# Kernel tuning notes

Measured on AMD Instinct MI355X. Metric: run time of the kernel, lower is better.

Reference implementation:

```python
import jax, jax.numpy as jnp
import numpy as np

B, N, E = 8, 1000, 16000
HIST, PRED = 8, 12
IN_DIM = 14          # pm25(1) + met features(13)
HID_GAT, HEADS = 256, 8
GNN_OUT = 13
HID = 64             # GRU hidden (self.hid_dim = 64 in source)


def setup_inputs() -> dict:
    key = jax.random.key(0)
    ks = jax.random.split(key, 20)
    p = lambda k, shp, s=0.05: jax.random.normal(k, shp, dtype=jnp.float32) * s
    return {
        "pm25_hist": jax.random.normal(ks[0], (B, HIST, N, 1), dtype=jnp.float32),
        "feature": jax.random.normal(ks[1], (B, HIST + PRED, N, IN_DIM - 1), dtype=jnp.float32),
        "edge_index": jax.random.randint(ks[2], (2, E), 0, N),
        "gat1_W": p(ks[3], (IN_DIM, HEADS * HID_GAT)),
        "gat1_att_src": p(ks[4], (HEADS, HID_GAT)),
        "gat1_att_dst": p(ks[5], (HEADS, HID_GAT)),
        "gat1_b": p(ks[6], (HEADS * HID_GAT,)),
        "gat2_W": p(ks[7], (HEADS * HID_GAT, GNN_OUT)),
        "gat2_att_src": p(ks[8], (1, GNN_OUT)),
        "gat2_att_dst": p(ks[9], (1, GNN_OUT)),
        "gat2_b": p(ks[10], (GNN_OUT,)),
        "gru_W_ih": p(ks[11], (3 * HID, IN_DIM + GNN_OUT)),
        "gru_W_hh": p(ks[12], (3 * HID, HID)),
        "gru_b_ih": p(ks[13], (3 * HID,)),
        "gru_b_hh": p(ks[14], (3 * HID,)),
        "fc_out_W": p(ks[15], (HID, 1)),
        "fc_out_b": p(ks[16], (1,)),
    }


def _gat_conv(x, W, a_src, a_dst, b, src, dst, concat):
    # Single-graph GATConv (PyG semantics, eval mode: dropout disabled).
    # x: [N, F_in]; src/dst: [E'] (self-loops already appended)
    H, D = a_src.shape
    h = (x @ W).reshape(N, H, D)                       # [N, H, D]
    e = jax.nn.leaky_relu(
        (h * a_src).sum(-1)[src] + (h * a_dst).sum(-1)[dst], 0.2
    )                                                  # [E', H]
    # segment softmax over incoming edges of each dst node
    m = jax.ops.segment_max(e, dst, num_segments=N)
    ex = jnp.exp(e - m[dst])
    alpha = ex / jax.ops.segment_sum(ex, dst, num_segments=N)[dst]
    out = jax.ops.segment_sum(alpha[:, :, None] * h[src], dst, num_segments=N)  # [N, H, D]
    return (out.reshape(N, H * D) + b) if concat else (out.mean(1) + b)


def reference(pm25_hist, feature, edge_index,
              gat1_W, gat1_att_src, gat1_att_dst, gat1_b,
              gat2_W, gat2_att_src, gat2_att_dst, gat2_b,
              gru_W_ih, gru_W_hh, gru_b_ih, gru_b_hh,
              fc_out_W, fc_out_b):
    # add self-loops (PyG GATConv default)
    loop = jnp.arange(N)
    src = jnp.concatenate([edge_index[0], loop])
    dst = jnp.concatenate([edge_index[1], loop])

    def gnn(x):  # x: [N, IN_DIM] -> [N, GNN_OUT]
        h = jax.nn.elu(_gat_conv(x, gat1_W, gat1_att_src, gat1_att_dst, gat1_b, src, dst, True))
        return _gat_conv(h, gat2_W, gat2_att_src, gat2_att_dst, gat2_b, src, dst, False)

    gnn_b = jax.vmap(gnn)

    def gru(x, h):  # torch.nn.GRUCell math
        i_r, i_z, i_n = jnp.split(x @ gru_W_ih.T + gru_b_ih, 3, axis=-1)
        h_r, h_z, h_n = jnp.split(h @ gru_W_hh.T + gru_b_hh, 3, axis=-1)
        r = jax.nn.sigmoid(i_r + h_r)
        z = jax.nn.sigmoid(i_z + h_z)
        n = jnp.tanh(i_n + r * h_n)
        return (1.0 - z) * n + z * h

    feats = jnp.moveaxis(feature[:, HIST:HIST + PRED], 1, 0)  # [PRED, B, N, 13]

    def step(carry, f_t):
        hn, xn = carry
        x = jnp.concatenate([xn, f_t], axis=-1)               # [B, N, IN_DIM]
        g = gnn_b(x)                                          # [B, N, GNN_OUT]
        gx = jnp.concatenate([g, x], axis=-1).reshape(B * N, IN_DIM + GNN_OUT)
        hn = gru(gx, hn)                                      # [B*N, HID]
        xn = hn.reshape(B, N, HID) @ fc_out_W + fc_out_b      # [B, N, 1]
        return (hn, xn), xn

    h0 = jnp.zeros((B * N, HID), jnp.float32)
    xn0 = pm25_hist[:, -1]                                    # [B, N, 1]
    _, preds = jax.lax.scan(step, (h0, xn0), feats)
    return jnp.moveaxis(preds, 0, 1)                          # [B, PRED, N, 1]
```

## Files before the change

### kernel.cpp

```cpp
#include <hip/hip_runtime.h>
#include <hip/hip_bf16.h>
#include <math.h>

#define BB 8
#define NN 1000
#define EE 16000
#define ETOT 17000
#define TPRED 12
#define FEAT 13
#define INDIM 14
#define HEADS 8
#define HG 256
#define C1 2048
#define GO 13
#define HID 64

typedef unsigned int  uint32;
typedef unsigned short ushort16;
typedef uint32 uvec4 __attribute__((ext_vector_type(4)));
typedef __fp16 hf2 __attribute__((ext_vector_type(2)));

union U32H2 { uint32 u; hf2 h; };
__device__ __forceinline__ hf2 u2h(uint32 u){ U32H2 c; c.u=u; return c.h; }
__device__ __forceinline__ uint32 h2u(hf2 h){ U32H2 c; c.h=h; return c.u; }

#if __has_builtin(__builtin_amdgcn_fdot2)
__device__ __forceinline__ float FDOT2(hf2 a, hf2 b, float c){
    return __builtin_amdgcn_fdot2(a, b, c, false);
}
#else
__device__ __forceinline__ float FDOT2(hf2 a, hf2 b, float c){
    return c + (float)a.x*(float)b.x + (float)a.y*(float)b.y;
}
#endif

__device__ __forceinline__ float lrelu(float v){ return v > 0.f ? v : 0.2f*v; }

__device__ __forceinline__ ushort16 f2bf(float f){
    union { float f; uint32 u; } v; v.f = f;
    uint32 r = v.u + 0x7FFFu + ((v.u >> 16) & 1u);
    return (ushort16)(r >> 16);
}
__device__ __forceinline__ uint32 pack2(float lo, float hi){
    return (uint32)f2bf(lo) | ((uint32)f2bf(hi) << 16);
}
__device__ __forceinline__ void cvt2(uint32 u, float& lo, float& hi){
    union { uint32 u; float f; } a, b;
    a.u = u << 16; b.u = u & 0xFFFF0000u;
    lo = a.f; hi = b.f;
}
__device__ __forceinline__ uint32 pkh(float lo, float hi){
    hf2 h; h.x = (__fp16)lo; h.y = (__fp16)hi; return h2u(h);
}

__global__ void k_prep(const float* W1, const float* a1s, const float* a1d,
                       const float* W2, const float* a2s, const float* a2d,
                       const float* Wih, const float* Whh,
                       float* Wsrc, float* Wdst, uint32* w1pk, uint32* w2pk,
                       uint32* WihP, uint32* WhhP){
    __shared__ float rs[4], rd[4];
    int bid = blockIdx.x, tid = threadIdx.x;
    if (bid < 112){
        int k = bid >> 3, h = bid & 7;
        float wv = W1[k*C1 + h*HG + tid];
        float ps = wv * a1s[h*HG + tid];
        float pd = wv * a1d[h*HG + tid];
        #pragma unroll
        for (int m=1;m<64;m<<=1){ ps += __shfl_xor(ps,m); pd += __shfl_xor(pd,m); }
        int w = tid>>6;
        if ((tid&63)==0){ rs[w]=ps; rd[w]=pd; }
        __syncthreads();
        if (tid==0){
            Wsrc[k*8+h] = rs[0]+rs[1]+rs[2]+rs[3];
            Wdst[k*8+h] = rd[0]+rd[1]+rd[2]+rd[3];
        }
    } else if (bid < 176){
        int i = (bid-112)*256 + tid;
        int c = i >> 3, kk = i & 7;
        float lo = (kk < 7) ? W1[(2*kk)*C1 + c]   : 0.f;
        float hi = (kk < 7) ? W1[(2*kk+1)*C1 + c] : 0.f;
        w1pk[i] = h2u(__builtin_amdgcn_cvt_pkrtz(lo, hi));
    } else if (bid < 180){
        int m = (bid-176)*256 + tid;
        if (m < C1/2){
            int c0 = 2*m, c1 = 2*m+1;
            float colA[16], colB[16];
            float ssA=0.f, ddA=0.f, ssB=0.f, ddB=0.f;
            #pragma unroll
            for (int j=0;j<GO;j++){
                float wA = W2[c0*GO+j], wB = W2[c1*GO+j];
                colA[j]=wA; colB[j]=wB;
                ssA += wA*a2s[j]; ddA += wA*a2d[j];
                ssB += wB*a2s[j]; ddB += wB*a2d[j];
            }
            colA[13]=ssA; colA[14]=ddA; colA[15]=0.f;
            colB[13]=ssB; colB[14]=ddB; colB[15]=0.f;
            #pragma unroll
            for (int j=0;j<16;j++)
                w2pk[m*16+j] = h2u(__builtin_amdgcn_cvt_pkrtz(colA[j], colB[j]));
        }
    } else {
        int i = (bid-180)*256 + tid;
        if (i < 192*14){
            int rr = i/14, c2 = i - rr*14;
            float lo = Wih[rr*27 + 2*c2];
            float hi = (2*c2+1 < 27) ? Wih[rr*27 + 2*c2 + 1] : 0.f;
            WihP[i] = pkh(lo, hi);
        }
        if (i < 192*32){
            int rr = i>>5, j2 = i&31;
            WhhP[i] = pkh(Whh[rr*64 + 2*j2], Whh[rr*64 + 2*j2 + 1]);
        }
    }
}

__global__ void k_init(const float* pm25, const float* feat,
                       const float* Wsrc, const float* Wdst,
                       float* hn, float* xn, int* count,
                       float* ssrc, float* sdst, uint32* xpk){
    int i = blockIdx.x*blockDim.x + threadIdx.x;
    if (i < BB*NN*HID) hn[i] = 0.f;
    if (i < NN) count[i] = 0;
    if (i < BB*NN){
        int b = i/NN, n = i%NN;
        float x[INDIM];
        x[0] = pm25[(b*8 + 7)*NN + n];
        xn[i] = x[0];
        const float* fp = feat + ((size_t)(b*20 + 8)*NN + n)*FEAT;
        #pragma unroll
        for (int k=0;k<FEAT;k++) x[k+1] = fp[k];
        #pragma unroll
        for (int h=0;h<8;h++){
            float ss=0.f, dd=0.f;
            #pragma unroll
            for (int k=0;k<INDIM;k++){ ss += x[k]*Wsrc[k*8+h]; dd += x[k]*Wdst[k*8+h]; }
            ssrc[i*8+h] = ss; sdst[i*8+h] = dd;
        }
        #pragma unroll
        for (int p=0;p<7;p++) xpk[i*8+p] = pack2(x[2*p], x[2*p+1]);
        xpk[i*8+7] = 0u;
    }
}

__global__ void k_count(const int* ei, int* count){
    int e = blockIdx.x*blockDim.x + threadIdx.x;
    if (e < ETOT){
        int dst = (e<EE) ? ei[EE+e] : (e-EE);
        atomicAdd(&count[dst], 1);
    }
}

__global__ void k_scan(const int* count, int* offs, int* cursor){
    __shared__ int s[1024];
    int tid = threadIdx.x;
    int myc = (tid<NN) ? count[tid] : 0;
    s[tid] = myc;
    __syncthreads();
    for (int d=1; d<1024; d<<=1){
        int v = (tid>=d) ? s[tid-d] : 0;
        __syncthreads();
        s[tid] += v;
        __syncthreads();
    }
    if (tid<NN){
        int off = s[tid] - myc;
        offs[tid] = off; cursor[tid] = off;
    }
    if (tid==NN-1) offs[NN] = s[tid];
}

__global__ void k_fill(const int* ei, int* cursor, int* csr_src){
    int e = blockIdx.x*blockDim.x + threadIdx.x;
    if (e < ETOT){
        int src = (e<EE) ? ei[e]    : (e-EE);
        int dst = (e<EE) ? ei[EE+e] : (e-EE);
        int pos = atomicAdd(&cursor[dst], 1);
        csr_src[pos] = src;
    }
}


__global__ __launch_bounds__(256) void k_gnn(const uint32* xpk, const float* ssrc,
        const float* sdst, const int* offs, const int* csr,
        const uint32* w1pk, const uint32* w2pk, const float* b1,
        float* h2o, float* s2s, float* s2d){
    int tid = threadIdx.x;
    int w = tid >> 6, lane = tid & 63;
    int hh = tid >> 5;
    uint32 w1r[64];
    #pragma unroll
    for (int q=0;q<16;q++){
        uvec4 u = *(const uvec4*)(w1pk + tid*64 + 4*q);
        w1r[4*q]=u.x; w1r[4*q+1]=u.y; w1r[4*q+2]=u.z; w1r[4*q+3]=u.w;
    }
    uint32 w2r[64];
    #pragma unroll
    for (int q=0;q<16;q++){
        uvec4 u = *(const uvec4*)(w2pk + tid*64 + 4*q);
        w2r[4*q]=u.x; w2r[4*q+1]=u.y; w2r[4*q+2]=u.z; w2r[4*q+3]=u.w;
    }
    float b1r[8];
    #pragma unroll
    for (int j=0;j<8;j++) b1r[j] = b1[8*tid+j];
    __shared__ float aggL[4][128];
    __shared__ float sred[256*17];
    __shared__ float red2[64];
    for (int rr=0; rr<4; rr++){
        int nid = rr*2048 + w*512 + blockIdx.x;
        if (nid < BB*NN){
            int b = nid & 7, dstn = nid >> 3;
            int bn = b*NN + dstn;
            int base = offs[dstn], deg = offs[dstn+1]-base;
            int slot = lane >> 3, h = lane & 7;
            float sdd = sdst[bn*8 + h];
            float mloc = -1e30f;
            for (int i=slot;i<deg;i+=8){
                int s = csr[base+i];
                mloc = fmaxf(mloc, lrelu(ssrc[(b*NN+s)*8+h]+sdd));
            }
            mloc = fmaxf(mloc, __shfl_xor(mloc,8));
            mloc = fmaxf(mloc, __shfl_xor(mloc,16));
            mloc = fmaxf(mloc, __shfl_xor(mloc,32));
            float dloc = 0.f;
            for (int i=slot;i<deg;i+=8){
                int s = csr[base+i];
                dloc += __expf(lrelu(ssrc[(b*NN+s)*8+h]+sdd)-mloc);
            }
            dloc += __shfl_xor(dloc,8); dloc += __shfl_xor(dloc,16); dloc += __shfl_xor(dloc,32);
            float rden = 1.f/dloc;
            float acc[14];
            #pragma unroll
            for (int k=0;k<14;k++) acc[k]=0.f;
            for (int i=slot;i<deg;i+=8){
                int s = csr[base+i];
                float al = __expf(lrelu(ssrc[(b*NN+s)*8+h]+sdd)-mloc)*rden;
                const uint32* xp = xpk + (size_t)(b*NN+s)*8;
                #pragma unroll
                for (int p=0;p<7;p++){
                    float x0,x1; cvt2(xp[p],x0,x1);
                    acc[2*p]   += al*x0;
                    acc[2*p+1] += al*x1;
                }
            }
            #pragma unroll
            for (int k=0;k<14;k++){
                acc[k] += __shfl_xor(acc[k],8);
                acc[k] += __shfl_xor(acc[k],16);
                acc[k] += __shfl_xor(acc[k],32);
            }
            if (slot==0){
                float* ag = &aggL[w][h*16];
                #pragma unroll
                for (int k=0;k<14;k++) ag[k] = acc[k];
            }
        }
        __syncthreads();
        #pragma unroll
        for (int i=0;i<4;i++){
            int nid2 = rr*2048 + i*512 + blockIdx.x;
            if (nid2 < BB*NN){
                int b2i = nid2 & 7, d2 = nid2 >> 3;
                int bn2 = b2i*NN + d2;
                const float4* ap = (const float4*)(&aggL[i][hh*16]);
                float4 A0=ap[0], A1=ap[1], A2=ap[2], A3=ap[3];
                hf2 agh[7];
                agh[0]=__builtin_amdgcn_cvt_pkrtz(A0.x,A0.y);
                agh[1]=__builtin_amdgcn_cvt_pkrtz(A0.z,A0.w);
                agh[2]=__builtin_amdgcn_cvt_pkrtz(A1.x,A1.y);
                agh[3]=__builtin_amdgcn_cvt_pkrtz(A1.z,A1.w);
                agh[4]=__builtin_amdgcn_cvt_pkrtz(A2.x,A2.y);
                agh[5]=__builtin_amdgcn_cvt_pkrtz(A2.z,A2.w);
                agh[6]=__builtin_amdgcn_cvt_pkrtz(A3.x,A3.y);
                float v[8];
                #pragma unroll
                for (int j=0;j<8;j++){
                    float s = b1r[j];
                    #pragma unroll
                    for (int kk=0;kk<7;kk++) s = FDOT2(agh[kk], u2h(w1r[j*8+kk]), s);
                    v[j] = s > 0.f ? s : __expf(s) - 1.f;
                }
                hf2 vp[4];
                #pragma unroll
                for (int q=0;q<4;q++) vp[q] = __builtin_amdgcn_cvt_pkrtz(v[2*q], v[2*q+1]);
                #pragma unroll
                for (int j=0;j<16;j++){
                    float s = 0.f;
                    #pragma unroll
                    for (int q=0;q<4;q++) s = FDOT2(vp[q], u2h(w2r[q*16+j]), s);
                    sred[tid*17 + j] = s;
                }
                __syncthreads();
                int j = tid & 15, g = tid >> 4;
                float s = 0.f;
                #pragma unroll
                for (int q=0;q<16;q++) s += sred[(g + 16*q)*17 + j];
                s += __shfl_xor(s, 16);
                s += __shfl_xor(s, 32);
                int ww = tid >> 6, ll = tid & 63;
                if (ll < 16) red2[ww*16 + ll] = s;
                __syncthreads();
                if (tid < 15){
                    float rv = red2[tid] + red2[16+tid] + red2[32+tid] + red2[48+tid];
                    if (tid < GO)      h2o[bn2*GO + tid] = rv;
                    else if (tid==13)  s2s[bn2] = rv;
                    else               s2d[bn2] = rv;
                }
                __syncthreads();
            }
        }
        __syncthreads();
    }
}

__global__ __launch_bounds__(64,2) void k_tail(int t, int last,
        const float* feat, const int* offs, const int* csr,
        const float* h2, const float* s2src, const float* s2dst, const float* b2,
        const uint32* WihP, const uint32* WhhP, const float* bih, const float* bhh,
        const float* fcw, const float* fcb, const float* Wsrc, const float* Wdst,
        float* hn, float* xn, float* out,
        float* ssrc, float* sdst, uint32* xpk){
    int lane = threadIdx.x;
    int slot = lane >> 4, cc = lane & 15;
    uint32 wih0[14], wih1[14], wih2[14];
    #pragma unroll
    for (int q=0;q<14;q++){
        wih0[q]=WihP[lane*14+q];
        wih1[q]=WihP[(64+lane)*14+q];
        wih2[q]=WihP[(128+lane)*14+q];
    }
    uint32 whh0[32], whh1[32], whh2[32];
    #pragma unroll
    for (int q=0;q<32;q++){
        whh0[q]=WhhP[lane*32+q];
        whh1[q]=WhhP[(64+lane)*32+q];
        whh2[q]=WhhP[(128+lane)*32+q];
    }
    float bi0=bih[lane], bi1=bih[64+lane], bi2=bih[128+lane];
    float bh0=bhh[lane], bh1=bhh[64+lane], bh2=bhh[128+lane];
    float fw = fcw[lane], fb = fcb[0];
    float b2c = b2[cc < GO ? cc : 0];
    __shared__ uint32 hsP[32];
    __shared__ float garr[14];
    for (int r=0;r<4;r++){
        int bn = blockIdx.x*4 + r;
        int b = bn/NN, n = bn - b*NN;
        int base = offs[n], deg = offs[n+1]-base;
        float sdd = s2dst[bn];
        float mloc = -1e30f;
        for (int e=slot;e<deg;e+=4){
            int s = csr[base+e];
            mloc = fmaxf(mloc, lrelu(s2src[b*NN+s] + sdd));
        }
        mloc = fmaxf(mloc, __shfl_xor(mloc,16));
        mloc = fmaxf(mloc, __shfl_xor(mloc,32));
        float dloc = 0.f;
        for (int e=slot;e<deg;e+=4){
            int s = csr[base+e];
            dloc += __expf(lrelu(s2src[b*NN+s] + sdd) - mloc);
        }
        dloc += __shfl_xor(dloc,16);
        dloc += __shfl_xor(dloc,32);
        float rdv = 1.f / dloc;
        float a = 0.f;
        for (int e=slot;e<deg;e+=4){
            int s = csr[base+e];
            float al = __expf(lrelu(s2src[b*NN+s] + sdd) - mloc) * rdv;
            a += al * h2[(size_t)(b*NN+s)*GO + cc];
        }
        a += __shfl_xor(a,16);
        a += __shfl_xor(a,32);
        float xnv = xn[bn];
        if (slot==0 && cc<GO)  garr[cc] = a + b2c;
        if (slot==0 && cc==GO) garr[GO] = xnv;
        float hold = hn[bn*HID + lane];
        if (lane<32) hsP[lane] = pkh(hn[bn*HID + 2*lane], hn[bn*HID + 2*lane + 1]);
        __syncthreads();
        const float* fp = feat + ((size_t)(b*20 + 8 + t)*NN + n)*FEAT;
        float ft[FEAT];
        #pragma unroll
        for (int k=0;k<FEAT;k++) ft[k] = fp[k];
        hf2 gx[14];
        #pragma unroll
        for (int p=0;p<7;p++) gx[p] = u2h(pkh(garr[2*p], garr[2*p+1]));
        #pragma unroll
        for (int p=0;p<6;p++) gx[7+p] = u2h(pkh(ft[2*p], ft[2*p+1]));
        gx[13] = u2h(pkh(ft[12], 0.f));
        float ir = bi0, iz = bi1, inn = bi2;
        #pragma unroll
        for (int c2=0;c2<14;c2++){
            ir  = FDOT2(gx[c2], u2h(wih0[c2]), ir);
            iz  = FDOT2(gx[c2], u2h(wih1[c2]), iz);
            inn = FDOT2(gx[c2], u2h(wih2[c2]), inn);
        }
        float hr = bh0, hz = bh1, hnv = bh2;
        #pragma unroll
        for (int j2=0;j2<32;j2++){
            hf2 hv = u2h(hsP[j2]);
            hr  = FDOT2(hv, u2h(whh0[j2]), hr);
            hz  = FDOT2(hv, u2h(whh1[j2]), hz);
            hnv = FDOT2(hv, u2h(whh2[j2]), hnv);
        }
        float rg = 1.f/(1.f+__expf(-(ir+hr)));
        float zg = 1.f/(1.f+__expf(-(iz+hz)));
        float nv = tanhf(inn + rg*hnv);
        float hnew = (1.f - zg)*nv + zg*hold;
        hn[bn*HID+lane] = hnew;
        float xv = hnew * fw;
        #pragma unroll
        for (int m=1;m<64;m<<=1) xv += __shfl_xor(xv,m);
        float res = xv + fb;
        if (lane==0){
            xn[bn] = res;
            out[(b*TPRED + t)*NN + n] = res;
        }
        if (!last){
            const float* fp2 = feat + ((size_t)(b*20 + 9 + t)*NN + n)*FEAT;
            if (lane < 16){
                int h = lane & 7;
                const float* Wa = (lane<8) ? Wsrc : Wdst;
                float s = res * Wa[h];
                #pragma unroll
                for (int k=1;k<14;k++) s += fp2[k-1]*Wa[k*8+h];
                if (lane<8) ssrc[bn*8+h] = s; else sdst[bn*8+h] = s;
            } else if (lane < 23){
                int p = lane - 16;
                float lo = (p==0) ? res : fp2[2*p-1];
                float hi = fp2[2*p];
                xpk[bn*8+p] = pack2(lo, hi);
            } else if (lane == 23){
                xpk[bn*8+7] = 0u;
            }
        }
        __syncthreads();
    }
}


extern "C" void kernel_launch(void* const* d_in, const int* in_sizes, int n_in,
                              void* d_out, int out_size, void* d_ws, size_t ws_size,
                              hipStream_t stream){
    const float* pm25 = (const float*)d_in[0];
    const float* feat = (const float*)d_in[1];
    const int*   ei   = (const int*)  d_in[2];
    const float* W1   = (const float*)d_in[3];
    const float* a1s  = (const float*)d_in[4];
    const float* a1d  = (const float*)d_in[5];
    const float* b1   = (const float*)d_in[6];
    const float* W2   = (const float*)d_in[7];
    const float* a2s  = (const float*)d_in[8];
    const float* a2d  = (const float*)d_in[9];
    const float* b2   = (const float*)d_in[10];
    const float* Wih  = (const float*)d_in[11];
    const float* Whh  = (const float*)d_in[12];
    const float* bih  = (const float*)d_in[13];
    const float* bhh  = (const float*)d_in[14];
    const float* fcw  = (const float*)d_in[15];
    const float* fcb  = (const float*)d_in[16];
    float* out = (float*)d_out;

    float* f = (float*)d_ws;
    size_t o = 0;
    float* ssrc1 = f+o; o += (size_t)BB*NN*8;
    float* sdst1 = f+o; o += (size_t)BB*NN*8;
    float* h2    = f+o; o += (size_t)BB*NN*GO + 8;
    float* s2s   = f+o; o += (size_t)BB*NN;
    float* s2d   = f+o; o += (size_t)BB*NN;
    float* hn    = f+o; o += (size_t)BB*NN*HID;
    float* xn    = f+o; o += (size_t)BB*NN;
    float* Wsrc  = f+o; o += INDIM*8;
    float* Wdst  = f+o; o += INDIM*8;
    uint32* xpk  = (uint32*)(f+o); o += (size_t)BB*NN*8;
    uint32* w1pk = (uint32*)(f+o); o += (size_t)C1*8;
    uint32* w2pk = (uint32*)(f+o); o += (size_t)(C1/2)*16;
    uint32* WihP = (uint32*)(f+o); o += 192*14;
    uint32* WhhP = (uint32*)(f+o); o += 192*32;
    int* ibase  = (int*)(f+o);
    int* count  = ibase;
    int* cursor = ibase + NN;
    int* offs   = ibase + 2*NN;
    int* csr    = ibase + 2*NN + NN + 1;

    k_prep  <<<204, 256,0,stream>>>(W1, a1s, a1d, W2, a2s, a2d, Wih, Whh,
                                    Wsrc, Wdst, w1pk, w2pk, WihP, WhhP);
    k_init  <<<2000,256,0,stream>>>(pm25, feat, Wsrc, Wdst, hn, xn, count,
                                    ssrc1, sdst1, xpk);
    k_count <<<67,  256,0,stream>>>(ei, count);
    k_scan  <<<1,  1024,0,stream>>>(count, offs, cursor);
    k_fill  <<<67,  256,0,stream>>>(ei, cursor, csr);

    for (int t=0; t<TPRED; t++){
        k_gnn  <<<512, 256,0,stream>>>(xpk, ssrc1, sdst1, offs, csr,
                                       w1pk, w2pk, b1, h2, s2s, s2d);
        k_tail <<<2000, 64,0,stream>>>(t, (t==TPRED-1)?1:0, feat, offs, csr,
                                       h2, s2s, s2d, b2,
                                       WihP, WhhP, bih, bhh, fcw, fcb, Wsrc, Wdst,
                                       hn, xn, out, ssrc1, sdst1, xpk);
    }
}
```

Measured before the change: 927.2 us.

## Split fused GAT kernel into separate aggregation and expansion kernels

The fused k_gnn kernel, which had each 256-thread block run both the edge-softmax aggregation and the weight-resident expansion, is split in two. k_agg14 runs one 64-thread block per (batch, node) to compute the 14-wide attention-weighted aggregates and writes them to a new global buffer. k_expand is a grid-stride kernel with 1024 blocks that keeps the packed weights in registers and applies the two GAT linear layers. The aim is to free the irregular gather phase from the register-heavy expansion's occupancy limit, at the cost of an extra kernel launch per step and a global round trip for the aggregates.

```diff
diff --git a/kernel.cpp b/kernel.cpp
--- a/kernel.cpp
+++ b/kernel.cpp
@@ -180,12 +180,63 @@
 }
 
 
-__global__ __launch_bounds__(256) void k_gnn(const uint32* xpk, const float* ssrc,
-        const float* sdst, const int* offs, const int* csr,
-        const uint32* w1pk, const uint32* w2pk, const float* b1,
-        float* h2o, float* s2s, float* s2d){
+__global__ __launch_bounds__(64) void k_agg14(const uint32* xpk, const float* ssrc,
+        const float* sdst, const int* offs, const int* csr, float* agg){
+    int lane = threadIdx.x;
+    int blk = blockIdx.x;
+    int b = blk & 7, dstn = blk >> 3;
+    int bn = b*NN + dstn;
+    int base = offs[dstn], deg = offs[dstn+1]-base;
+    int slot = lane >> 3, h = lane & 7;
+    float sdd = sdst[bn*8 + h];
+    float mloc = -1e30f;
+    for (int i=slot;i<deg;i+=8){
+        int s = csr[base+i];
+        mloc = fmaxf(mloc, lrelu(ssrc[(b*NN+s)*8+h]+sdd));
+    }
+    mloc = fmaxf(mloc, __shfl_xor(mloc,8));
+    mloc = fmaxf(mloc, __shfl_xor(mloc,16));
+    mloc = fmaxf(mloc, __shfl_xor(mloc,32));
+    float dloc = 0.f;
+    for (int i=slot;i<deg;i+=8){
+        int s = csr[base+i];
+        dloc += __expf(lrelu(ssrc[(b*NN+s)*8+h]+sdd)-mloc);
+    }
+    dloc += __shfl_xor(dloc,8); dloc += __shfl_xor(dloc,16); dloc += __shfl_xor(dloc,32);
+    float rden = 1.f/dloc;
+    float acc[14];
+    #pragma unroll
+    for (int k=0;k<14;k++) acc[k]=0.f;
+    for (int i=slot;i<deg;i+=8){
+        int s = csr[base+i];
+        float al = __expf(lrelu(ssrc[(b*NN+s)*8+h]+sdd)-mloc)*rden;
+        const uint32* xp = xpk + (size_t)(b*NN+s)*8;
+        #pragma unroll
+        for (int p=0;p<7;p++){
+            float x0,x1; cvt2(xp[p],x0,x1);
+            acc[2*p]   += al*x0;
+            acc[2*p+1] += al*x1;
+        }
+    }
+    #pragma unroll
+    for (int k=0;k<14;k++){
+        acc[k] += __shfl_xor(acc[k],8);
+        acc[k] += __shfl_xor(acc[k],16);
+        acc[k] += __shfl_xor(acc[k],32);
+    }
+    if (slot==0){
+        float* ag = agg + (size_t)bn*128 + h*16;
+        #pragma unroll
+        for (int p=0;p<7;p++){
+            float2 st; st.x = acc[2*p]; st.y = acc[2*p+1];
+            *(float2*)(ag + 2*p) = st;
+        }
+    }
+}
+
+__global__ __launch_bounds__(256,1) void k_expand(const float* agg, const uint32* w1pk,
+        const uint32* w2pk, const float* b1, float* h2o, float* s2s, float* s2d){
     int tid = threadIdx.x;
-    int w = tid >> 6, lane = tid & 63;
     int hh = tid >> 5;
     uint32 w1r[64];
     #pragma unroll
@@ -202,111 +253,52 @@
     float b1r[8];
     #pragma unroll
     for (int j=0;j<8;j++) b1r[j] = b1[8*tid+j];
-    __shared__ float aggL[4][128];
     __shared__ float sred[256*17];
     __shared__ float red2[64];
-    for (int rr=0; rr<4; rr++){
-        int nid = rr*2048 + w*512 + blockIdx.x;
-        if (nid < BB*NN){
-            int b = nid & 7, dstn = nid >> 3;
-            int bn = b*NN + dstn;
-            int base = offs[dstn], deg = offs[dstn+1]-base;
-            int slot = lane >> 3, h = lane & 7;
-            float sdd = sdst[bn*8 + h];
-            float mloc = -1e30f;
-            for (int i=slot;i<deg;i+=8){
-                int s = csr[base+i];
-                mloc = fmaxf(mloc, lrelu(ssrc[(b*NN+s)*8+h]+sdd));
-            }
-            mloc = fmaxf(mloc, __shfl_xor(mloc,8));
-            mloc = fmaxf(mloc, __shfl_xor(mloc,16));
-            mloc = fmaxf(mloc, __shfl_xor(mloc,32));
-            float dloc = 0.f;
-            for (int i=slot;i<deg;i+=8){
-                int s = csr[base+i];
-                dloc += __expf(lrelu(ssrc[(b*NN+s)*8+h]+sdd)-mloc);
-            }
-            dloc += __shfl_xor(dloc,8); dloc += __shfl_xor(dloc,16); dloc += __shfl_xor(dloc,32);
-            float rden = 1.f/dloc;
-            float acc[14];
+    for (int idx = blockIdx.x; idx < BB*NN; idx += gridDim.x){
+        const float4* ap = (const float4*)(agg + (size_t)idx*128 + hh*16);
+        float4 A0=ap[0], A1=ap[1], A2=ap[2], A3=ap[3];
+        hf2 agh[7];
+        agh[0]=__builtin_amdgcn_cvt_pkrtz(A0.x,A0.y);
+        agh[1]=__builtin_amdgcn_cvt_pkrtz(A0.z,A0.w);
+        agh[2]=__builtin_amdgcn_cvt_pkrtz(A1.x,A1.y);
+        agh[3]=__builtin_amdgcn_cvt_pkrtz(A1.z,A1.w);
+        agh[4]=__builtin_amdgcn_cvt_pkrtz(A2.x,A2.y);
+        agh[5]=__builtin_amdgcn_cvt_pkrtz(A2.z,A2.w);
+        agh[6]=__builtin_amdgcn_cvt_pkrtz(A3.x,A3.y);
+        float v[8];
+        #pragma unroll
+        for (int j=0;j<8;j++){
+            float s = b1r[j];
             #pragma unroll
-            for (int k=0;k<14;k++) acc[k]=0.f;
-            for (int i=slot;i<deg;i+=8){
-                int s = csr[base+i];
-                float al = __expf(lrelu(ssrc[(b*NN+s)*8+h]+sdd)-mloc)*rden;
-                const uint32* xp = xpk + (size_t)(b*NN+s)*8;
-                #pragma unroll
-                for (int p=0;p<7;p++){
-                    float x0,x1; cvt2(xp[p],x0,x1);
-                    acc[2*p]   += al*x0;
-                    acc[2*p+1] += al*x1;
-                }
-            }
+            for (int kk=0;kk<7;kk++) s = FDOT2(agh[kk], u2h(w1r[j*8+kk]), s);
+            v[j] = s > 0.f ? s : __expf(s) - 1.f;
+        }
+        hf2 vp[4];
+        #pragma unroll
+        for (int q=0;q<4;q++) vp[q] = __builtin_amdgcn_cvt_pkrtz(v[2*q], v[2*q+1]);
+        #pragma unroll
+        for (int j=0;j<16;j++){
+            float s = 0.f;
             #pragma unroll
-            for (int k=0;k<14;k++){
-                acc[k] += __shfl_xor(acc[k],8);
-                acc[k] += __shfl_xor(acc[k],16);
-                acc[k] += __shfl_xor(acc[k],32);
-            }
-            if (slot==0){
-                float* ag = &aggL[w][h*16];
-                #pragma unroll
-                for (int k=0;k<14;k++) ag[k] = acc[k];
-            }
-        }
-        __syncthreads();
-        #pragma unroll
-        for (int i=0;i<4;i++){
-            int nid2 = rr*2048 + i*512 + blockIdx.x;
-            if (nid2 < BB*NN){
-                int b2i = nid2 & 7, d2 = nid2 >> 3;
-                int bn2 = b2i*NN + d2;
-                const float4* ap = (const float4*)(&aggL[i][hh*16]);
-                float4 A0=ap[0], A1=ap[1], A2=ap[2], A3=ap[3];
-                hf2 agh[7];
-                agh[0]=__builtin_amdgcn_cvt_pkrtz(A0.x,A0.y);
-                agh[1]=__builtin_amdgcn_cvt_pkrtz(A0.z,A0.w);
-                agh[2]=__builtin_amdgcn_cvt_pkrtz(A1.x,A1.y);
-                agh[3]=__builtin_amdgcn_cvt_pkrtz(A1.z,A1.w);
-                agh[4]=__builtin_amdgcn_cvt_pkrtz(A2.x,A2.y);
-                agh[5]=__builtin_amdgcn_cvt_pkrtz(A2.z,A2.w);
-                agh[6]=__builtin_amdgcn_cvt_pkrtz(A3.x,A3.y);
-                float v[8];
-                #pragma unroll
-                for (int j=0;j<8;j++){
-                    float s = b1r[j];
-                    #pragma unroll
-                    for (int kk=0;kk<7;kk++) s = FDOT2(agh[kk], u2h(w1r[j*8+kk]), s);
-                    v[j] = s > 0.f ? s : __expf(s) - 1.f;
-                }
-                hf2 vp[4];
-                #pragma unroll
-                for (int q=0;q<4;q++) vp[q] = __builtin_amdgcn_cvt_pkrtz(v[2*q], v[2*q+1]);
-                #pragma unroll
-                for (int j=0;j<16;j++){
-                    float s = 0.f;
-                    #pragma unroll
-                    for (int q=0;q<4;q++) s = FDOT2(vp[q], u2h(w2r[q*16+j]), s);
-                    sred[tid*17 + j] = s;
-                }
-                __syncthreads();
-                int j = tid & 15, g = tid >> 4;
-                float s = 0.f;
-                #pragma unroll
-                for (int q=0;q<16;q++) s += sred[(g + 16*q)*17 + j];
-                s += __shfl_xor(s, 16);
-                s += __shfl_xor(s, 32);
-                int ww = tid >> 6, ll = tid & 63;
-                if (ll < 16) red2[ww*16 + ll] = s;
-                __syncthreads();
-                if (tid < 15){
-                    float rv = red2[tid] + red2[16+tid] + red2[32+tid] + red2[48+tid];
-                    if (tid < GO)      h2o[bn2*GO + tid] = rv;
-                    else if (tid==13)  s2s[bn2] = rv;
-                    else               s2d[bn2] = rv;
-                }
-                __syncthreads();
-            }
+            for (int q=0;q<4;q++) s = FDOT2(vp[q], u2h(w2r[q*16+j]), s);
+            sred[tid*17 + j] = s;
+        }
+        __syncthreads();
+        int j = tid & 15, g = tid >> 4;
+        float s = 0.f;
+        #pragma unroll
+        for (int i=0;i<16;i++) s += sred[(g + 16*i)*17 + j];
+        s += __shfl_xor(s, 16);
+        s += __shfl_xor(s, 32);
+        int lane = tid & 63, w = tid >> 6;
+        if (lane < 16) red2[w*16 + lane] = s;
+        __syncthreads();
+        if (tid < 15){
+            float r = red2[tid] + red2[16+tid] + red2[32+tid] + red2[48+tid];
+            if (tid < GO)      h2o[idx*GO + tid] = r;
+            else if (tid==13)  s2s[idx] = r;
+            else               s2d[idx] = r;
         }
         __syncthreads();
     }
@@ -462,6 +454,7 @@
     size_t o = 0;
     float* ssrc1 = f+o; o += (size_t)BB*NN*8;
     float* sdst1 = f+o; o += (size_t)BB*NN*8;
+    float* agg   = f+o; o += (size_t)BB*NN*128;
     float* h2    = f+o; o += (size_t)BB*NN*GO + 8;
     float* s2s   = f+o; o += (size_t)BB*NN;
     float* s2d   = f+o; o += (size_t)BB*NN;
@@ -489,11 +482,11 @@
     k_fill  <<<67,  256,0,stream>>>(ei, cursor, csr);
 
     for (int t=0; t<TPRED; t++){
-        k_gnn  <<<512, 256,0,stream>>>(xpk, ssrc1, sdst1, offs, csr,
-                                       w1pk, w2pk, b1, h2, s2s, s2d);
-        k_tail <<<2000, 64,0,stream>>>(t, (t==TPRED-1)?1:0, feat, offs, csr,
-                                       h2, s2s, s2d, b2,
-                                       WihP, WhhP, bih, bhh, fcw, fcb, Wsrc, Wdst,
-                                       hn, xn, out, ssrc1, sdst1, xpk);
-    }
-}
+        k_agg14 <<<8000, 64,0,stream>>>(xpk, ssrc1, sdst1, offs, csr, agg);
+        k_expand<<<1024,256,0,stream>>>(agg, w1pk, w2pk, b1, h2, s2s, s2d);
+        k_tail  <<<2000, 64,0,stream>>>(t, (t==TPRED-1)?1:0, feat, offs, csr,
+                                        h2, s2s, s2d, b2,
+                                        WihP, WhhP, bih, bhh, fcw, fcb, Wsrc, Wdst,
+                                        hn, xn, out, ssrc1, sdst1, xpk);
+    }
+}
```

Measured after the change: 965.3 us. 1.04x slower.
